# Performance work log

Measured on AMD Instinct MI355X. Metric: run time of the kernel, lower is better.

## Reference

```python
import jax, jax.numpy as jnp
import numpy as np

D = 1024  # model dimension

def _linear_params(key, d_in, d_out):
    kw, kb = jax.random.split(key)
    bound = 1.0 / np.sqrt(d_in)
    W = jax.random.uniform(kw, (d_out, d_in), minval=-bound, maxval=bound, dtype=jnp.float32)
    b = jax.random.uniform(kb, (d_out,), minval=-bound, maxval=bound, dtype=jnp.float32)
    return W, b

def setup_inputs() -> dict:
    key = jax.random.key(0)
    kx, ki, kq, kk, kv, ko = jax.random.split(key, 6)
    B, S = 4, 2048
    X = jax.random.normal(kx, (B, S, D), dtype=jnp.float32)
    intensity = jax.random.uniform(ki, (B, S, S), dtype=jnp.float32)
    Wq, bq = _linear_params(kq, D, D)
    Wk, bk = _linear_params(kk, D, D)
    Wv, bv = _linear_params(kv, D, D)
    Wo, bo = _linear_params(ko, D, D)
    return {"X": X, "intensity": intensity,
            "Wq": Wq, "bq": bq, "Wk": Wk, "bk": bk,
            "Wv": Wv, "bv": bv, "Wo": Wo, "bo": bo}

def reference(X, intensity, Wq, bq, Wk, bk, Wv, bv, Wo, bo):
    d_k = Wq.shape[0]
    q = X @ Wq.T + bq                      # [B,S,D]
    k = X @ Wk.T + bk                      # [B,S,D]
    v = X @ Wv.T + bv                      # [B,S,D]
    scores = jnp.einsum('bsd,btd->bst', q, k) / jnp.sqrt(jnp.asarray(d_k, X.dtype))
    attn = jax.nn.softmax(scores, axis=-1) + intensity  # non-standard additive epilogue
    out = jnp.einsum('bst,btd->bsd', attn, v)
    return out @ Wo.T + bo
```

## Files before the change

kernel.cpp:

```cpp
#include <hip/hip_runtime.h>

typedef __attribute__((ext_vector_type(8))) short bf16x8;
typedef __attribute__((ext_vector_type(4))) float f32x4;

__device__ __forceinline__ unsigned short f2bf(float f) {
  union { float f; unsigned u; } a; a.f = f;
  unsigned u = a.u;
  unsigned r = (u + 0x7FFFu + ((u >> 16) & 1u)) >> 16;
  return (unsigned short)r;
}

__device__ __forceinline__ void stage16(const void* g, void* l) {
  __builtin_amdgcn_global_load_lds((const __attribute__((address_space(1))) unsigned int*)g,
                                   (__attribute__((address_space(3))) unsigned int*)l,
                                   16, 0, 0);
}

template<bool OUT_BF16, int BIAS_MODE>
__global__ __launch_bounds__(256) void gemm_nt(
    const unsigned short* __restrict__ A,
    const unsigned short* __restrict__ B,
    void* __restrict__ Cv,
    const float* __restrict__ bias,
    float scale, int K,
    int lda, int ldb, int ldc,
    long batchA, long batchB, long batchC)
{
  __shared__ __attribute__((aligned(16))) unsigned short lsA[128 * 32];
  __shared__ __attribute__((aligned(16))) unsigned short lsB[128 * 32];

  const int tid  = threadIdx.x;
  const int lane = tid & 63;
  const int wid  = tid >> 6;
  const long bz  = blockIdx.z;
  A += bz * batchA;
  B += bz * batchB;
  const int tileM = blockIdx.x * 128;
  const int tileN = blockIdx.y * 128;

  const int sr = tid >> 2;
  const int sc = (tid & 3) << 3;
  const unsigned short* gA0 = A + (size_t)(tileM + sr) * lda + sc;
  const unsigned short* gA1 = A + (size_t)(tileM + 64 + sr) * lda + sc;
  const unsigned short* gB0 = B + (size_t)(tileN + sr) * ldb + sc;
  const unsigned short* gB1 = B + (size_t)(tileN + 64 + sr) * ldb + sc;
  unsigned short* dA0 = &lsA[tid * 8];
  unsigned short* dA1 = &lsA[2048 + tid * 8];
  unsigned short* dB0 = &lsB[tid * 8];
  unsigned short* dB1 = &lsB[2048 + tid * 8];

  f32x4 acc[4][4];
#pragma unroll
  for (int m = 0; m < 4; ++m)
#pragma unroll
    for (int n = 0; n < 4; ++n) acc[m][n] = (f32x4){0.f, 0.f, 0.f, 0.f};

  const int wr = (wid >> 1) << 6;
  const int wc = (wid & 1) << 6;
  const unsigned short* pa = &lsA[(wr + (lane & 15)) * 32 + ((lane >> 4) << 3)];
  const unsigned short* pb = &lsB[(wc + (lane & 15)) * 32 + ((lane >> 4) << 3)];

  for (int k0 = 0; k0 < K; k0 += 32) {
    stage16(gA0 + k0, dA0);
    stage16(gA1 + k0, dA1);
    stage16(gB0 + k0, dB0);
    stage16(gB1 + k0, dB1);
    __syncthreads();

    bf16x8 af[4], bfr[4];
#pragma unroll
    for (int m = 0; m < 4; ++m) af[m]  = *(const bf16x8*)(pa + m * 16 * 32);
#pragma unroll
    for (int n = 0; n < 4; ++n) bfr[n] = *(const bf16x8*)(pb + n * 16 * 32);
#pragma unroll
    for (int m = 0; m < 4; ++m)
#pragma unroll
      for (int n = 0; n < 4; ++n)
        acc[m][n] = __builtin_amdgcn_mfma_f32_16x16x32_bf16(af[m], bfr[n], acc[m][n], 0, 0, 0);
    __syncthreads();
  }

  const int ro = (lane >> 4) << 2;
  const int co = lane & 15;
#pragma unroll
  for (int m = 0; m < 4; ++m) {
#pragma unroll
    for (int n = 0; n < 4; ++n) {
      const int row0 = tileM + wr + m * 16 + ro;
      const int col  = tileN + wc + n * 16 + co;
#pragma unroll
      for (int r = 0; r < 4; ++r) {
        float v = acc[m][n][r] * scale;
        const int row = row0 + r;
        if (BIAS_MODE == 1) v += bias[col];
        if (BIAS_MODE == 2) v += bias[row];
        const size_t ci = (size_t)(bz * batchC) + (size_t)row * ldc + col;
        if (OUT_BF16) ((unsigned short*)Cv)[ci] = f2bf(v);
        else          ((float*)Cv)[ci] = v;
      }
    }
  }
}

__global__ __launch_bounds__(256) void softmax_add_bf16(
    float* __restrict__ scores, const float* __restrict__ inten)
{
  const int row = blockIdx.x;
  float* srow = scores + (size_t)row * 2048;
  const float* irow = inten + (size_t)row * 2048;
  const int t = threadIdx.x;
  const int lane = t & 63, wid = t >> 6;

  float v[8];
  float mx = -3.4e38f;
#pragma unroll
  for (int j = 0; j < 8; ++j) { v[j] = srow[t + j * 256]; mx = fmaxf(mx, v[j]); }

  __shared__ float red[8];
#pragma unroll
  for (int o = 32; o; o >>= 1) mx = fmaxf(mx, __shfl_xor(mx, o));
  if (lane == 0) red[wid] = mx;
  __syncthreads();
  mx = fmaxf(fmaxf(red[0], red[1]), fmaxf(red[2], red[3]));

  float s = 0.f;
#pragma unroll
  for (int j = 0; j < 8; ++j) { v[j] = __expf(v[j] - mx); s += v[j]; }
#pragma unroll
  for (int o = 32; o; o >>= 1) s += __shfl_xor(s, o);
  if (lane == 0) red[4 + wid] = s;
  __syncthreads();
  s = red[4] + red[5] + red[6] + red[7];
  const float inv = 1.f / s;

  unsigned short* arow = (unsigned short*)srow;
#pragma unroll
  for (int j = 0; j < 8; ++j)
    arow[t + j * 256] = f2bf(v[j] * inv + irow[t + j * 256]);
}

__global__ __launch_bounds__(256) void cvt_bf16(
    const float* __restrict__ in, unsigned short* __restrict__ out, int n)
{
  const int i = (blockIdx.x * 256 + threadIdx.x) * 4;
  if (i >= n) return;
  const float4 f = *(const float4*)(in + i);
  ushort4 o;
  o.x = f2bf(f.x); o.y = f2bf(f.y); o.z = f2bf(f.z); o.w = f2bf(f.w);
  *(ushort4*)(out + i) = o;
}

extern "C" void kernel_launch(void* const* d_in, const int* in_sizes, int n_in,
                              void* d_out, int out_size, void* d_ws, size_t ws_size,
                              hipStream_t stream)
{
  const float* X     = (const float*)d_in[0];
  const float* inten = (const float*)d_in[1];
  const float* Wq = (const float*)d_in[2];
  const float* bq = (const float*)d_in[3];
  const float* Wk = (const float*)d_in[4];
  const float* bk = (const float*)d_in[5];
  const float* Wv = (const float*)d_in[6];
  const float* bv = (const float*)d_in[7];
  const float* Wo = (const float*)d_in[8];
  const float* bo = (const float*)d_in[9];
  float* out = (float*)d_out;

  const int B = 4, S = 2048, D = 1024;
  const int MS = B * S;
  char* ws = (char*)d_ws;
  const size_t MB = 1 << 20;
  unsigned short* Xb  = (unsigned short*)(ws);
  unsigned short* Wqb = (unsigned short*)(ws + 16 * MB);
  unsigned short* Wkb = (unsigned short*)(ws + 18 * MB);
  unsigned short* Wvb = (unsigned short*)(ws + 20 * MB);
  unsigned short* Wob = (unsigned short*)(ws + 22 * MB);
  unsigned short* Q   = (unsigned short*)(ws + 24 * MB);
  unsigned short* Kb  = (unsigned short*)(ws + 40 * MB);
  unsigned short* Vt  = (unsigned short*)(ws + 56 * MB);
  unsigned short* Oa  = (unsigned short*)(ws + 72 * MB);
  float*          Sc  = (float*)(ws + 88 * MB);

  cvt_bf16<<<(MS * D) / 1024, 256, 0, stream>>>(X,  Xb,  MS * D);
  cvt_bf16<<<(D * D) / 1024, 256, 0, stream>>>(Wq, Wqb, D * D);
  cvt_bf16<<<(D * D) / 1024, 256, 0, stream>>>(Wk, Wkb, D * D);
  cvt_bf16<<<(D * D) / 1024, 256, 0, stream>>>(Wv, Wvb, D * D);
  cvt_bf16<<<(D * D) / 1024, 256, 0, stream>>>(Wo, Wob, D * D);

  dim3 gproj(MS / 128, D / 128, 1);
  gemm_nt<true, 1><<<gproj, 256, 0, stream>>>(Xb, Wqb, Q,  bq, 1.f, D, D, D, D, 0, 0, 0);
  gemm_nt<true, 1><<<gproj, 256, 0, stream>>>(Xb, Wkb, Kb, bk, 1.f, D, D, D, D, 0, 0, 0);

  dim3 gvt(D / 128, S / 128, B);
  gemm_nt<true, 2><<<gvt, 256, 0, stream>>>(Wvb, Xb, Vt, bv, 1.f, D, D, D, S,
                                            0, (long)S * D, (long)D * S);

  dim3 gsc(S / 128, S / 128, B);
  gemm_nt<false, 0><<<gsc, 256, 0, stream>>>(Q, Kb, Sc, nullptr, 0.03125f, D,
                                             D, D, S,
                                             (long)S * D, (long)S * D, (long)S * S);

  softmax_add_bf16<<<B * S, 256, 0, stream>>>(Sc, inten);

  dim3 gav(S / 128, D / 128, B);
  gemm_nt<true, 0><<<gav, 256, 0, stream>>>((unsigned short*)Sc, Vt, Oa, nullptr,
                                            1.f, S, 2 * S, S, D,
                                            (long)S * 2 * S, (long)D * S, (long)S * D);

  gemm_nt<false, 1><<<gproj, 256, 0, stream>>>(Oa, Wob, out, bo, 1.f, D, D, D, D, 0, 0, 0);
}
```

Measured before the change: 424.4 us.

## Restructure GEMM with triple-buffered LDS pipeline, swizzle, larger tiles and XCD remap

Rewrites the shared GEMM kernel to use 256x128 tiles with 512 threads and a K step of 64. It triple-buffers the LDS tiles in dynamic shared memory so global-to-LDS loads for step t+2 overlap the MFMA work on step t, and uses XOR-swizzled LDS addressing to avoid bank conflicts. Blocks are remapped round-robin across the 8 XCDs to improve L2 locality, and MFMA issue priority is raised around the compute section. The costs are 144KB of LDS per block, which limits occupancy to one block per CU, and hand-written vmcnt waits that must stay in step with the number of outstanding loads.

Result: faster. 349.8 us (-17.6%).

```diff
diff --git a/kernel.cpp b/kernel.cpp
--- a/kernel.cpp
+++ b/kernel.cpp
@@ -2,6 +2,10 @@
 
 typedef __attribute__((ext_vector_type(8))) short bf16x8;
 typedef __attribute__((ext_vector_type(4))) float f32x4;
+
+#define LDS_TILE (48 * 1024)
+#define NBUF 3
+#define LDS_TOTAL (NBUF * LDS_TILE)
 
 __device__ __forceinline__ unsigned short f2bf(float f) {
   union { float f; unsigned u; } a; a.f = f;
@@ -17,7 +21,7 @@
 }
 
 template<bool OUT_BF16, int BIAS_MODE>
-__global__ __launch_bounds__(256) void gemm_nt(
+__global__ __launch_bounds__(512) void gemm_nt(
     const unsigned short* __restrict__ A,
     const unsigned short* __restrict__ B,
     void* __restrict__ Cv,
@@ -26,28 +30,42 @@
     int lda, int ldb, int ldc,
     long batchA, long batchB, long batchC)
 {
-  __shared__ __attribute__((aligned(16))) unsigned short lsA[128 * 32];
-  __shared__ __attribute__((aligned(16))) unsigned short lsB[128 * 32];
+  extern __shared__ char smem[];
+
+  const int gx = gridDim.x, gy = gridDim.y;
+  int bid = blockIdx.x + gx * (blockIdx.y + gy * blockIdx.z);
+  const int nwg = gx * gy * gridDim.z;
+  const int q = nwg >> 3;
+  int wg = (bid & 7) * q + (bid >> 3);
+  const int tx = wg % gx;
+  int rest = wg / gx;
+  const int ty = rest % gy;
+  const int tz = rest / gy;
 
   const int tid  = threadIdx.x;
   const int lane = tid & 63;
   const int wid  = tid >> 6;
-  const long bz  = blockIdx.z;
-  A += bz * batchA;
-  B += bz * batchB;
-  const int tileM = blockIdx.x * 128;
-  const int tileN = blockIdx.y * 128;
-
-  const int sr = tid >> 2;
-  const int sc = (tid & 3) << 3;
-  const unsigned short* gA0 = A + (size_t)(tileM + sr) * lda + sc;
-  const unsigned short* gA1 = A + (size_t)(tileM + 64 + sr) * lda + sc;
-  const unsigned short* gB0 = B + (size_t)(tileN + sr) * ldb + sc;
-  const unsigned short* gB1 = B + (size_t)(tileN + 64 + sr) * ldb + sc;
-  unsigned short* dA0 = &lsA[tid * 8];
-  unsigned short* dA1 = &lsA[2048 + tid * 8];
-  unsigned short* dB0 = &lsB[tid * 8];
-  unsigned short* dB1 = &lsB[2048 + tid * 8];
+  const int wm   = wid & 3;
+  const int wn   = wid >> 2;
+
+  A += (long)tz * batchA;
+  B += (long)tz * batchB;
+  const int tileM = tx * 256;
+  const int tileN = ty * 128;
+
+  const int srow = tid >> 3;
+  const int scol = (((tid & 7) ^ (srow & 7)) << 3);
+  const unsigned short* ga[4];
+  const unsigned short* gb[2];
+#pragma unroll
+  for (int j = 0; j < 4; ++j) ga[j] = A + (size_t)(tileM + j * 64 + srow) * lda + scol;
+#pragma unroll
+  for (int j = 0; j < 2; ++j) gb[j] = B + (size_t)(tileN + j * 64 + srow) * ldb + scol;
+
+  const int frow  = lane & 15;
+  const int k0slot = (lane >> 4) ^ (lane & 7);
+  const int aoff = (wm * 64 + frow) * 128;
+  const int boff = 32768 + (wn * 64 + frow) * 128;
 
   f32x4 acc[4][4];
 #pragma unroll
@@ -55,30 +73,61 @@
 #pragma unroll
     for (int n = 0; n < 4; ++n) acc[m][n] = (f32x4){0.f, 0.f, 0.f, 0.f};
 
-  const int wr = (wid >> 1) << 6;
-  const int wc = (wid & 1) << 6;
-  const unsigned short* pa = &lsA[(wr + (lane & 15)) * 32 + ((lane >> 4) << 3)];
-  const unsigned short* pb = &lsB[(wc + (lane & 15)) * 32 + ((lane >> 4) << 3)];
-
-  for (int k0 = 0; k0 < K; k0 += 32) {
-    stage16(gA0 + k0, dA0);
-    stage16(gA1 + k0, dA1);
-    stage16(gB0 + k0, dB0);
-    stage16(gB1 + k0, dB1);
-    __syncthreads();
-
-    bf16x8 af[4], bfr[4];
-#pragma unroll
-    for (int m = 0; m < 4; ++m) af[m]  = *(const bf16x8*)(pa + m * 16 * 32);
-#pragma unroll
-    for (int n = 0; n < 4; ++n) bfr[n] = *(const bf16x8*)(pb + n * 16 * 32);
-#pragma unroll
-    for (int m = 0; m < 4; ++m)
-#pragma unroll
-      for (int n = 0; n < 4; ++n)
-        acc[m][n] = __builtin_amdgcn_mfma_f32_16x16x32_bf16(af[m], bfr[n], acc[m][n], 0, 0, 0);
-    __syncthreads();
+  const int nt = K >> 6;
+
+#define STAGE(t)                                                         \
+  do {                                                                   \
+    char* d_ = smem + ((t) % NBUF) * LDS_TILE;                           \
+    const int kc_ = (t) << 6;                                            \
+    _Pragma("unroll")                                                    \
+    for (int j = 0; j < 4; ++j) stage16(ga[j] + kc_, d_ + j * 8192 + tid * 16); \
+    _Pragma("unroll")                                                    \
+    for (int j = 0; j < 2; ++j) stage16(gb[j] + kc_, d_ + 32768 + j * 8192 + tid * 16); \
+  } while (0)
+
+#define COMPUTE(t)                                                       \
+  do {                                                                   \
+    const char* d_ = smem + ((t) % NBUF) * LDS_TILE;                     \
+    bf16x8 af[4][2], bfr[4][2];                                          \
+    _Pragma("unroll")                                                    \
+    for (int ks = 0; ks < 2; ++ks) {                                     \
+      const int so_ = ((k0slot ^ (ks << 2)) << 4);                       \
+      _Pragma("unroll")                                                  \
+      for (int m = 0; m < 4; ++m)                                        \
+        af[m][ks] = *(const bf16x8*)(d_ + aoff + m * 2048 + so_);        \
+      _Pragma("unroll")                                                  \
+      for (int n = 0; n < 4; ++n)                                        \
+        bfr[n][ks] = *(const bf16x8*)(d_ + boff + n * 2048 + so_);       \
+    }                                                                    \
+    __builtin_amdgcn_s_setprio(1);                                       \
+    _Pragma("unroll")                                                    \
+    for (int ks = 0; ks < 2; ++ks)                                       \
+      _Pragma("unroll")                                                  \
+      for (int m = 0; m < 4; ++m)                                        \
+        _Pragma("unroll")                                                \
+        for (int n = 0; n < 4; ++n)                                      \
+          acc[m][n] = __builtin_amdgcn_mfma_f32_16x16x32_bf16(af[m][ks], bfr[n][ks], acc[m][n], 0, 0, 0); \
+    __builtin_amdgcn_s_setprio(0);                                       \
+  } while (0)
+
+  STAGE(0);
+  STAGE(1);
+  asm volatile("s_waitcnt vmcnt(6)" ::: "memory");
+  __builtin_amdgcn_s_barrier();
+
+  for (int t = 0; t < nt - 2; ++t) {
+    STAGE(t + 2);
+    COMPUTE(t);
+    asm volatile("s_waitcnt vmcnt(6)" ::: "memory");
+    __builtin_amdgcn_s_barrier();
   }
+  COMPUTE(nt - 2);
+  asm volatile("s_waitcnt vmcnt(0)" ::: "memory");
+  __builtin_amdgcn_s_barrier();
+  COMPUTE(nt - 1);
+
+#undef STAGE
+#undef COMPUTE
 
   const int ro = (lane >> 4) << 2;
   const int co = lane & 15;
@@ -86,15 +135,15 @@
   for (int m = 0; m < 4; ++m) {
 #pragma unroll
     for (int n = 0; n < 4; ++n) {
-      const int row0 = tileM + wr + m * 16 + ro;
-      const int col  = tileN + wc + n * 16 + co;
+      const int row0 = tileM + wm * 64 + m * 16 + ro;
+      const int col  = tileN + wn * 64 + n * 16 + co;
 #pragma unroll
       for (int r = 0; r < 4; ++r) {
         float v = acc[m][n][r] * scale;
         const int row = row0 + r;
         if (BIAS_MODE == 1) v += bias[col];
         if (BIAS_MODE == 2) v += bias[row];
-        const size_t ci = (size_t)(bz * batchC) + (size_t)row * ldc + col;
+        const size_t ci = (size_t)(tz * batchC) + (size_t)row * ldc + col;
         if (OUT_BF16) ((unsigned short*)Cv)[ci] = f2bf(v);
         else          ((float*)Cv)[ci] = v;
       }
@@ -181,31 +230,37 @@
   unsigned short* Oa  = (unsigned short*)(ws + 72 * MB);
   float*          Sc  = (float*)(ws + 88 * MB);
 
+  hipFuncSetAttribute((const void*)gemm_nt<true, 1>,  hipFuncAttributeMaxDynamicSharedMemorySize, LDS_TOTAL);
+  hipFuncSetAttribute((const void*)gemm_nt<true, 2>,  hipFuncAttributeMaxDynamicSharedMemorySize, LDS_TOTAL);
+  hipFuncSetAttribute((const void*)gemm_nt<false, 0>, hipFuncAttributeMaxDynamicSharedMemorySize, LDS_TOTAL);
+  hipFuncSetAttribute((const void*)gemm_nt<true, 0>,  hipFuncAttributeMaxDynamicSharedMemorySize, LDS_TOTAL);
+  hipFuncSetAttribute((const void*)gemm_nt<false, 1>, hipFuncAttributeMaxDynamicSharedMemorySize, LDS_TOTAL);
+
   cvt_bf16<<<(MS * D) / 1024, 256, 0, stream>>>(X,  Xb,  MS * D);
   cvt_bf16<<<(D * D) / 1024, 256, 0, stream>>>(Wq, Wqb, D * D);
   cvt_bf16<<<(D * D) / 1024, 256, 0, stream>>>(Wk, Wkb, D * D);
   cvt_bf16<<<(D * D) / 1024, 256, 0, stream>>>(Wv, Wvb, D * D);
   cvt_bf16<<<(D * D) / 1024, 256, 0, stream>>>(Wo, Wob, D * D);
 
-  dim3 gproj(MS / 128, D / 128, 1);
-  gemm_nt<true, 1><<<gproj, 256, 0, stream>>>(Xb, Wqb, Q,  bq, 1.f, D, D, D, D, 0, 0, 0);
-  gemm_nt<true, 1><<<gproj, 256, 0, stream>>>(Xb, Wkb, Kb, bk, 1.f, D, D, D, D, 0, 0, 0);
-
-  dim3 gvt(D / 128, S / 128, B);
-  gemm_nt<true, 2><<<gvt, 256, 0, stream>>>(Wvb, Xb, Vt, bv, 1.f, D, D, D, S,
-                                            0, (long)S * D, (long)D * S);
-
-  dim3 gsc(S / 128, S / 128, B);
-  gemm_nt<false, 0><<<gsc, 256, 0, stream>>>(Q, Kb, Sc, nullptr, 0.03125f, D,
-                                             D, D, S,
-                                             (long)S * D, (long)S * D, (long)S * S);
+  dim3 gproj(MS / 256, D / 128, 1);
+  gemm_nt<true, 1><<<gproj, 512, LDS_TOTAL, stream>>>(Xb, Wqb, Q,  bq, 1.f, D, D, D, D, 0, 0, 0);
+  gemm_nt<true, 1><<<gproj, 512, LDS_TOTAL, stream>>>(Xb, Wkb, Kb, bk, 1.f, D, D, D, D, 0, 0, 0);
+
+  dim3 gvt(D / 256, S / 128, B);
+  gemm_nt<true, 2><<<gvt, 512, LDS_TOTAL, stream>>>(Wvb, Xb, Vt, bv, 1.f, D, D, D, S,
+                                                    0, (long)S * D, (long)D * S);
+
+  dim3 gsc(S / 256, S / 128, B);
+  gemm_nt<false, 0><<<gsc, 512, LDS_TOTAL, stream>>>(Q, Kb, Sc, nullptr, 0.03125f, D,
+                                                     D, D, S,
+                                                     (long)S * D, (long)S * D, (long)S * S);
 
   softmax_add_bf16<<<B * S, 256, 0, stream>>>(Sc, inten);
 
-  dim3 gav(S / 128, D / 128, B);
-  gemm_nt<true, 0><<<gav, 256, 0, stream>>>((unsigned short*)Sc, Vt, Oa, nullptr,
-                                            1.f, S, 2 * S, S, D,
-                                            (long)S * 2 * S, (long)D * S, (long)S * D);
-
-  gemm_nt<false, 1><<<gproj, 256, 0, stream>>>(Oa, Wob, out, bo, 1.f, D, D, D, D, 0, 0, 0);
-}
+  dim3 gav(S / 256, D / 128, B);
+  gemm_nt<true, 0><<<gav, 512, LDS_TOTAL, stream>>>((unsigned short*)Sc, Vt, Oa, nullptr,
+                                                    1.f, S, 2 * S, S, D,
+                                                    (long)S * 2 * S, (long)D * S, (long)S * D);
+
+  gemm_nt<false, 1><<<gproj, 512, LDS_TOTAL, stream>>>(Oa, Wob, out, bo, 1.f, D, D, D, D, 0, 0, 0);
+}
```
